# Performance work log

Measured on AMD Instinct MI355X. Metric: run time of the kernel, lower is better.

## Reference

```python
import jax, jax.numpy as jnp
import numpy as np

B, H, S, D = 4, 16, 2048, 128
D_MODEL = 128  # scale factor per module init


def setup_inputs() -> dict:
    key = jax.random.key(0)
    kq, kk, kv = jax.random.split(key, 3)
    Q = jax.random.normal(kq, (B, H, S, D), dtype=jnp.float32)
    K = jax.random.normal(kk, (B, H, S, D), dtype=jnp.float32)
    V = jax.random.normal(kv, (B, H, S, D), dtype=jnp.float32)
    return {"Q": Q, "K": K, "V": V}


def reference(Q, K, V):
    # scores: [B, H, S, S]
    scores = jnp.einsum("bhqd,bhkd->bhqk", Q, K) / np.sqrt(D_MODEL).astype(np.float32)
    # causal mask: lower-triangular keeps, upper becomes -inf
    q_idx = jnp.arange(S)[:, None]
    k_idx = jnp.arange(S)[None, :]
    causal = q_idx >= k_idx  # [S, S]
    scores = jnp.where(causal, scores, -jnp.inf)
    attn = jax.nn.softmax(scores, axis=-1)
    return jnp.einsum("bhqk,bhkd->bhqd", attn, V)
```

## Files before the change

kernel.cpp:

```cpp
#include <hip/hip_runtime.h>

typedef _Float16 f16;
typedef _Float16 f16x8 __attribute__((ext_vector_type(8)));
typedef float    f32x16 __attribute__((ext_vector_type(16)));
typedef int      i32x4 __attribute__((ext_vector_type(4)));

#define B_ 4
#define H_ 16
#define S_ 2048
#define D_ 128
#define KVB 32
#define KSTR 136
#define VTSTR 40

union U4 { i32x4 i; f16x8 h; };

__device__ __forceinline__ unsigned pk2(float a, float b) {
    auto v = __builtin_amdgcn_cvt_pkrtz(a, b);
    return __builtin_bit_cast(unsigned, v);
}

__device__ __forceinline__ f16x8 cvt8(const float4 a, const float4 b) {
    f16x8 h;
    h[0] = (f16)a.x; h[1] = (f16)a.y; h[2] = (f16)a.z; h[3] = (f16)a.w;
    h[4] = (f16)b.x; h[5] = (f16)b.y; h[6] = (f16)b.z; h[7] = (f16)b.w;
    return h;
}

__global__ __launch_bounds__(256)
void prep(const float* __restrict__ K, const float* __restrict__ V,
          f16* __restrict__ Kh, f16* __restrict__ Vtt)
{
    const int bid = blockIdx.x;
    const int bh  = bid >> 5;
    const int kb  = bid & 31;
    const int k0  = kb * 64;
    const int tid = threadIdx.x;

    const float* Kb = K + ((size_t)bh * S_ + k0) * D_;
    const float* Vb = V + ((size_t)bh * S_ + k0) * D_;
    f16* Khb = Kh + ((size_t)bh * S_ + k0) * D_;
    f16* Vtb = Vtt + (size_t)bh * S_ * D_ + (size_t)kb * 2 * (D_ * 32);

    #pragma unroll
    for (int it = 0; it < 4; ++it) {
        const int idx = tid + it * 256;
        const int row = idx >> 4, c8 = idx & 15;
        const float4 a = *(const float4*)(Kb + row * D_ + c8 * 8);
        const float4 b = *(const float4*)(Kb + row * D_ + c8 * 8 + 4);
        *(f16x8*)(Khb + row * D_ + c8 * 8) = cvt8(a, b);
    }
    #pragma unroll
    for (int it = 0; it < 4; ++it) {
        const int idx = tid + it * 256;
        const int d  = idx & 127;
        const int k8 = idx >> 7;
        const float* vp = Vb + (size_t)(k8 * 8) * D_ + d;
        f16x8 vh;
        #pragma unroll
        for (int e = 0; e < 8; ++e) vh[e] = (f16)vp[(size_t)e * D_];
        *(f16x8*)(Vtb + (size_t)(k8 >> 2) * (D_ * 32) + d * 32 + (k8 & 3) * 8) = vh;
    }
}

__global__ __launch_bounds__(256, 2)
void fattn10(const float* __restrict__ Qg, const f16* __restrict__ Khg,
             const f16* __restrict__ Vttg, float* __restrict__ Og)
{
    __shared__ __align__(16) f16 Klds[2][KVB * KSTR];
    __shared__ __align__(16) f16 Vt[2][128 * VTSTR];

    const int id  = blockIdx.x;
    const int xcd = id & 7;
    const int r   = id >> 3;
    const int bh  = xcd + 8 * (r & 7);
    const int p   = r >> 3;

    const int tid  = threadIdx.x;
    const int lane = tid & 63;
    const int l31  = lane & 31;
    const int h    = lane >> 5;
    const int wv   = tid >> 6;

    const float* Qb  = Qg   + (size_t)bh * S_ * D_;
    const f16*   Khb = Khg  + (size_t)bh * S_ * D_;
    const f16*   Vtb = Vttg + (size_t)bh * S_ * D_;
    float*       Ob  = Og   + (size_t)bh * S_ * D_;

    i32x4 kr[2], vr[2];
    auto issue = [&](int kt) {
        const int k0n = kt * KVB;
        #pragma unroll
        for (int it = 0; it < 2; ++it) {
            const int idx  = tid + it * 256;
            const int krow = idx >> 4, c8 = idx & 15;
            kr[it] = *(const i32x4*)(Khb + (size_t)(k0n + krow) * D_ + c8 * 8);
            vr[it] = *(const i32x4*)(Vtb + (size_t)kt * (D_ * 32) + (size_t)idx * 8);
        }
    };
    auto writeLds = [&](int buf) {
        #pragma unroll
        for (int it = 0; it < 2; ++it) {
            const int idx  = tid + it * 256;
            const int krow = idx >> 4, c8 = idx & 15;
            *(i32x4*)&Klds[buf][krow * KSTR + c8 * 8] = kr[it];
            const int d = idx >> 2, kk8 = idx & 3;
            *(i32x4*)&Vt[buf][d * VTSTR + kk8 * 8] = vr[it];
        }
    };
    f16x8 qf[8];
    auto qkt = [&](int buf) {
        f32x16 a;
        #pragma unroll
        for (int rr = 0; rr < 16; ++rr) a[rr] = 0.f;
        #pragma unroll
        for (int dc = 0; dc < 8; ++dc) {
            const f16x8 kf = *(const f16x8*)&Klds[buf][l31 * KSTR + dc * 16 + h * 8];
            a = __builtin_amdgcn_mfma_f32_32x32x16_f16(kf, qf[dc], a, 0, 0, 0);
        }
        return a;
    };

    const float qmul = 0.08838834764831845f * 1.4426950408889634f;

    #pragma unroll 1
    for (int ph = 0; ph < 2; ++ph) {
        const int qt  = ph ? 15 - p : p;
        const int qw0 = qt * 128 + wv * 32;
        const int qg  = qw0 + l31;
        const int nkt = 4 * qt + 4;

        issue(0);
        {
            const float* Qrow = Qb + (size_t)(qw0 + l31) * D_;
            #pragma unroll
            for (int dc = 0; dc < 8; ++dc) {
                const float4 a = *(const float4*)(Qrow + dc * 16 + h * 8);
                const float4 b = *(const float4*)(Qrow + dc * 16 + h * 8 + 4);
                f16x8 q;
                q[0] = (f16)(a.x * qmul); q[1] = (f16)(a.y * qmul);
                q[2] = (f16)(a.z * qmul); q[3] = (f16)(a.w * qmul);
                q[4] = (f16)(b.x * qmul); q[5] = (f16)(b.y * qmul);
                q[6] = (f16)(b.z * qmul); q[7] = (f16)(b.w * qmul);
                qf[dc] = q;
            }
        }

        f32x16 acc[4];
        #pragma unroll
        for (int dt = 0; dt < 4; ++dt)
            #pragma unroll
            for (int rr = 0; rr < 16; ++rr) acc[dt][rr] = 0.f;
        float m_i = -1e30f, l_i = 0.f;

        __syncthreads();
        writeLds(0);
        issue(1);
        __syncthreads();

        f32x16 sv = qkt(0);

        for (int kt = 0; kt < nkt; ++kt) {
            const int cur  = kt & 1;
            const bool more = (kt + 1 < nkt);

            if (more) {
                __syncthreads();
                writeLds(cur ^ 1);
                if (kt + 2 < nkt) issue(kt + 2);
                __syncthreads();
            }

            __builtin_amdgcn_s_setprio(1);
            f32x16 svn;
            if (more) svn = qkt(cur ^ 1);

            const int k0 = kt * KVB;
            if (k0 + 31 > qw0) {
                #pragma unroll
                for (int rr = 0; rr < 16; ++rr) {
                    const int kg = k0 + (rr & 3) + 8 * (rr >> 2) + 4 * h;
                    if (kg > qg) sv[rr] = -1e30f;
                }
            }
            float t[8];
            #pragma unroll
            for (int rr = 0; rr < 8; ++rr) t[rr] = fmaxf(sv[2 * rr], sv[2 * rr + 1]);
            #pragma unroll
            for (int rr = 0; rr < 4; ++rr) t[rr] = fmaxf(t[rr], t[rr + 4]);
            t[0] = fmaxf(t[0], t[2]); t[1] = fmaxf(t[1], t[3]);
            float mx = fmaxf(t[0], t[1]);
            mx = fmaxf(mx, __shfl_xor(mx, 32));
            if (!__all(mx - m_i <= 8.0f)) {
                const float mn = fmaxf(m_i, mx);
                const float al = exp2f(m_i - mn);
                m_i = mn;
                l_i *= al;
                float arow[16];
                #pragma unroll
                for (int rr = 0; rr < 16; ++rr)
                    arow[rr] = __shfl(al, (rr & 3) + 8 * (rr >> 2) + 4 * h);
                #pragma unroll
                for (int dt = 0; dt < 4; ++dt)
                    #pragma unroll
                    for (int rr = 0; rr < 16; ++rr) acc[dt][rr] *= arow[rr];
            }
            #pragma unroll
            for (int rr = 0; rr < 16; ++rr) sv[rr] = exp2f(sv[rr] - m_i);
            float s8[8];
            #pragma unroll
            for (int rr = 0; rr < 8; ++rr) s8[rr] = sv[2 * rr] + sv[2 * rr + 1];
            #pragma unroll
            for (int rr = 0; rr < 4; ++rr) s8[rr] += s8[rr + 4];
            s8[0] += s8[2]; s8[1] += s8[3];
            float rs = s8[0] + s8[1];
            rs += __shfl_xor(rs, 32);
            l_i += rs;
            U4 pa[2];
            {
                unsigned dwp[8];
                #pragma unroll
                for (int m = 0; m < 8; ++m) dwp[m] = pk2(sv[2 * m], sv[2 * m + 1]);
                #pragma unroll
                for (int hf = 0; hf < 2; ++hf) {
                    const unsigned a0 = dwp[hf * 4 + 0], a1 = dwp[hf * 4 + 1];
                    const unsigned b0 = dwp[hf * 4 + 2], b1 = dwp[hf * 4 + 3];
                    const unsigned sa0 = (unsigned)__shfl_xor((int)a0, 32);
                    const unsigned sa1 = (unsigned)__shfl_xor((int)a1, 32);
                    const unsigned sb0 = (unsigned)__shfl_xor((int)b0, 32);
                    const unsigned sb1 = (unsigned)__shfl_xor((int)b1, 32);
                    i32x4 d;
                    d[0] = h ? (int)sb0 : (int)a0;
                    d[1] = h ? (int)sb1 : (int)a1;
                    d[2] = h ? (int)b0  : (int)sa0;
                    d[3] = h ? (int)b1  : (int)sa1;
                    pa[hf].i = d;
                }
            }
            #pragma unroll
            for (int dt = 0; dt < 4; ++dt) {
                const f16* vrow = &Vt[cur][(dt * 32 + l31) * VTSTR + h * 8];
                const f16x8 vb0 = *(const f16x8*)(vrow + 0);
                const f16x8 vb1 = *(const f16x8*)(vrow + 16);
                acc[dt] = __builtin_amdgcn_mfma_f32_32x32x16_f16(pa[0].h, vb0, acc[dt], 0, 0, 0);
                acc[dt] = __builtin_amdgcn_mfma_f32_32x32x16_f16(pa[1].h, vb1, acc[dt], 0, 0, 0);
            }
            __builtin_amdgcn_s_setprio(0);

            if (more) sv = svn;
        }

        float li[16];
        #pragma unroll
        for (int rr = 0; rr < 16; ++rr) {
            const float lv = __shfl(l_i, (rr & 3) + 8 * (rr >> 2) + 4 * h);
            li[rr] = 1.0f / lv;
        }
        #pragma unroll
        for (int dt = 0; dt < 4; ++dt)
            #pragma unroll
            for (int rr = 0; rr < 16; ++rr) {
                const int row = qw0 + (rr & 3) + 8 * (rr >> 2) + 4 * h;
                Ob[(size_t)row * D_ + dt * 32 + l31] = acc[dt][rr] * li[rr];
            }
    }
}

__global__ __launch_bounds__(256, 3)
void fattn5(const float* __restrict__ Qg, const float* __restrict__ Kg,
            const float* __restrict__ Vg, float* __restrict__ Og)
{
    __shared__ __align__(16) f16 Klds[2][KVB * KSTR];
    __shared__ __align__(16) f16 Vt[2][128 * VTSTR];
    const int id  = blockIdx.x;
    const int xcd = id & 7;
    const int w   = id >> 3;
    const int qt  = 15 - (w & 15);
    const int bh  = xcd + 8 * (w >> 4);
    const int tid  = threadIdx.x;
    const int lane = tid & 63;
    const int wv   = tid >> 6;
    const int l31  = lane & 31;
    const int h    = lane >> 5;
    const int qw0 = qt * 128 + wv * 32;
    const int qg  = qw0 + l31;
    const size_t base = (size_t)bh * S_ * D_;
    const float* Qb = Qg + base;
    const float* Kb = Kg + base;
    const float* Vb = Vg + base;
    float*       Ob = Og + base;
    const int nkt = 4 * qt + 4;
    float4 kr[4];
    float  vr[16];
    auto issue = [&](int kt) {
        const int k0n = kt * KVB;
        #pragma unroll
        for (int it = 0; it < 2; ++it) {
            const int idx  = tid + it * 256;
            const int krow = idx >> 4;
            const int c8   = idx & 15;
            const float* kp = Kb + (size_t)(k0n + krow) * D_ + c8 * 8;
            kr[it * 2]     = *(const float4*)kp;
            kr[it * 2 + 1] = *(const float4*)(kp + 4);
            const int d  = idx & 127;
            const int k8 = idx >> 7;
            const float* vp = Vb + (size_t)(k0n + k8 * 8) * D_ + d;
            #pragma unroll
            for (int e = 0; e < 8; ++e) vr[it * 8 + e] = vp[(size_t)e * D_];
        }
    };
    auto writeLds = [&](int buf) {
        #pragma unroll
        for (int it = 0; it < 2; ++it) {
            const int idx  = tid + it * 256;
            const int krow = idx >> 4;
            const int c8   = idx & 15;
            *(f16x8*)&Klds[buf][krow * KSTR + c8 * 8] = cvt8(kr[it * 2], kr[it * 2 + 1]);
            const int d  = idx & 127;
            const int k8 = idx >> 7;
            f16x8 vh;
            #pragma unroll
            for (int e = 0; e < 8; ++e) vh[e] = (f16)vr[it * 8 + e];
            *(f16x8*)&Vt[buf][d * VTSTR + k8 * 8] = vh;
        }
    };
    const float qmul = 0.08838834764831845f * 1.4426950408889634f;
    f16x8 qf[8];
    {
        const float* Qrow = Qb + (size_t)(qw0 + l31) * D_;
        #pragma unroll
        for (int dc = 0; dc < 8; ++dc) {
            const float4 a = *(const float4*)(Qrow + dc * 16 + h * 8);
            const float4 b = *(const float4*)(Qrow + dc * 16 + h * 8 + 4);
            f16x8 q;
            q[0] = (f16)(a.x * qmul); q[1] = (f16)(a.y * qmul);
            q[2] = (f16)(a.z * qmul); q[3] = (f16)(a.w * qmul);
            q[4] = (f16)(b.x * qmul); q[5] = (f16)(b.y * qmul);
            q[6] = (f16)(b.z * qmul); q[7] = (f16)(b.w * qmul);
            qf[dc] = q;
        }
    }
    f32x16 acc[4];
    #pragma unroll
    for (int dt = 0; dt < 4; ++dt)
        #pragma unroll
        for (int rr = 0; rr < 16; ++rr) acc[dt][rr] = 0.f;
    float m_i = -1e30f, l_i = 0.f;
    issue(0);
    writeLds(0);
    if (nkt > 1) issue(1);
    __syncthreads();
    for (int kt = 0; kt < nkt; ++kt) {
        const int k0  = kt * KVB;
        const int cur = kt & 1;
        if (k0 <= qw0 + 31) {
            f32x16 sv;
            #pragma unroll
            for (int rr = 0; rr < 16; ++rr) sv[rr] = 0.f;
            #pragma unroll
            for (int dc = 0; dc < 8; ++dc) {
                const f16x8 kf = *(const f16x8*)&Klds[cur][l31 * KSTR + dc * 16 + h * 8];
                sv = __builtin_amdgcn_mfma_f32_32x32x16_f16(kf, qf[dc], sv, 0, 0, 0);
            }
            if (k0 + 31 > qw0) {
                #pragma unroll
                for (int rr = 0; rr < 16; ++rr) {
                    const int kg = k0 + (rr & 3) + 8 * (rr >> 2) + 4 * h;
                    if (kg > qg) sv[rr] = -1e30f;
                }
            }
            float mx = sv[0];
            #pragma unroll
            for (int rr = 1; rr < 16; ++rr) mx = fmaxf(mx, sv[rr]);
            mx = fmaxf(mx, __shfl_xor(mx, 32));
            if (!__all(mx - m_i <= 8.0f)) {
                const float mn = fmaxf(m_i, mx);
                const float al = exp2f(m_i - mn);
                m_i = mn;
                l_i *= al;
                float arow[16];
                #pragma unroll
                for (int rr = 0; rr < 16; ++rr)
                    arow[rr] = __shfl(al, (rr & 3) + 8 * (rr >> 2) + 4 * h);
                #pragma unroll
                for (int dt = 0; dt < 4; ++dt)
                    #pragma unroll
                    for (int rr = 0; rr < 16; ++rr) acc[dt][rr] *= arow[rr];
            }
            float rs = 0.f;
            #pragma unroll
            for (int rr = 0; rr < 16; ++rr) {
                sv[rr] = exp2f(sv[rr] - m_i);
                rs += sv[rr];
            }
            rs += __shfl_xor(rs, 32);
            l_i += rs;
            U4 pa[2];
            {
                unsigned dwp[8];
                #pragma unroll
                for (int m = 0; m < 8; ++m) dwp[m] = pk2(sv[2 * m], sv[2 * m + 1]);
                #pragma unroll
                for (int hf = 0; hf < 2; ++hf) {
                    const unsigned a0 = dwp[hf * 4 + 0], a1 = dwp[hf * 4 + 1];
                    const unsigned b0 = dwp[hf * 4 + 2], b1 = dwp[hf * 4 + 3];
                    const unsigned sa0 = (unsigned)__shfl_xor((int)a0, 32);
                    const unsigned sa1 = (unsigned)__shfl_xor((int)a1, 32);
                    const unsigned sb0 = (unsigned)__shfl_xor((int)b0, 32);
                    const unsigned sb1 = (unsigned)__shfl_xor((int)b1, 32);
                    i32x4 d;
                    d[0] = h ? (int)sb0 : (int)a0;
                    d[1] = h ? (int)sb1 : (int)a1;
                    d[2] = h ? (int)b0  : (int)sa0;
                    d[3] = h ? (int)b1  : (int)sa1;
                    pa[hf].i = d;
                }
            }
            #pragma unroll
            for (int dt = 0; dt < 4; ++dt) {
                const f16* vrow = &Vt[cur][(dt * 32 + l31) * VTSTR + h * 8];
                const f16x8 vb0 = *(const f16x8*)(vrow + 0);
                const f16x8 vb1 = *(const f16x8*)(vrow + 16);
                acc[dt] = __builtin_amdgcn_mfma_f32_32x32x16_f16(pa[0].h, vb0, acc[dt], 0, 0, 0);
                acc[dt] = __builtin_amdgcn_mfma_f32_32x32x16_f16(pa[1].h, vb1, acc[dt], 0, 0, 0);
            }
        }
        if (kt + 1 < nkt) {
            writeLds(cur ^ 1);
            if (kt + 2 < nkt) issue(kt + 2);
            __syncthreads();
        }
    }
    float li[16];
    #pragma unroll
    for (int rr = 0; rr < 16; ++rr) {
        const float lv = __shfl(l_i, (rr & 3) + 8 * (rr >> 2) + 4 * h);
        li[rr] = 1.0f / lv;
    }
    #pragma unroll
    for (int dt = 0; dt < 4; ++dt)
        #pragma unroll
        for (int rr = 0; rr < 16; ++rr) {
            const int row = qw0 + (rr & 3) + 8 * (rr >> 2) + 4 * h;
            Ob[(size_t)row * D_ + dt * 32 + l31] = acc[dt][rr] * li[rr];
        }
}

extern "C" void kernel_launch(void* const* d_in, const int* in_sizes, int n_in,
                              void* d_out, int out_size, void* d_ws, size_t ws_size,
                              hipStream_t stream) {
    (void)in_sizes; (void)n_in; (void)out_size;
    const float* Q = (const float*)d_in[0];
    const float* K = (const float*)d_in[1];
    const float* V = (const float*)d_in[2];
    float* O = (float*)d_out;
    const size_t elems  = (size_t)B_ * H_ * S_ * D_;
    const size_t needKV = elems * 2 * sizeof(f16);
    if (ws_size >= needKV) {
        f16* Kh  = (f16*)d_ws;
        f16* Vtt = Kh + elems;
        prep<<<dim3(B_ * H_ * (S_ / 64)), dim3(256), 0, stream>>>(K, V, Kh, Vtt);
        fattn10<<<dim3(512), dim3(256), 0, stream>>>(Q, Kh, Vtt, O);
    } else {
        fattn5<<<dim3((S_ / 128) * B_ * H_), dim3(256), 0, stream>>>(Q, K, V, O);
    }
}
```

Measured before the change: 160.9 us.

## Skip fully masked causal tiles per wave and raise occupancy target

Each wave now works out the last KV tile its 32 query rows can see. It skips the QK^T MFMA and the whole softmax/PV block for tiles beyond that, while still taking part in the shared LDS loads and barriers. Launch bounds go from 2 to 3 blocks per SM, load and store addressing is precomputed outside the loop, the max reduction is reshaped into 3-input fmax chains, and the Q load loop is only partly unrolled to relieve register pressure. The aim is to drop wasted masked-tile work and improve latency hiding, at the risk of register spills under the tighter occupancy bound.

```diff
diff --git a/kernel.cpp b/kernel.cpp
--- a/kernel.cpp
+++ b/kernel.cpp
@@ -63,8 +63,8 @@
     }
 }
 
-__global__ __launch_bounds__(256, 2)
-void fattn10(const float* __restrict__ Qg, const f16* __restrict__ Khg,
+__global__ __launch_bounds__(256, 3)
+void fattn11(const float* __restrict__ Qg, const f16* __restrict__ Khg,
              const f16* __restrict__ Vttg, float* __restrict__ Og)
 {
     __shared__ __align__(16) f16 Klds[2][KVB * KSTR];
@@ -87,26 +87,27 @@
     const f16*   Vtb = Vttg + (size_t)bh * S_ * D_;
     float*       Ob  = Og   + (size_t)bh * S_ * D_;
 
+    const f16* kS = Khb + (tid >> 4) * D_ + (tid & 15) * 8;
+    const f16* vS = Vtb + (size_t)tid * 8;
+    const int  kDo = (tid >> 4) * KSTR + (tid & 15) * 8;
+    const int  vDo = (tid >> 2) * VTSTR + (tid & 3) * 8;
+
     i32x4 kr[2], vr[2];
     auto issue = [&](int kt) {
-        const int k0n = kt * KVB;
-        #pragma unroll
-        for (int it = 0; it < 2; ++it) {
-            const int idx  = tid + it * 256;
-            const int krow = idx >> 4, c8 = idx & 15;
-            kr[it] = *(const i32x4*)(Khb + (size_t)(k0n + krow) * D_ + c8 * 8);
-            vr[it] = *(const i32x4*)(Vtb + (size_t)kt * (D_ * 32) + (size_t)idx * 8);
-        }
+        const f16* kp = kS + ((size_t)kt << 12);
+        const f16* vp = vS + ((size_t)kt << 12);
+        kr[0] = *(const i32x4*)kp;
+        kr[1] = *(const i32x4*)(kp + 2048);
+        vr[0] = *(const i32x4*)vp;
+        vr[1] = *(const i32x4*)(vp + 2048);
     };
     auto writeLds = [&](int buf) {
-        #pragma unroll
-        for (int it = 0; it < 2; ++it) {
-            const int idx  = tid + it * 256;
-            const int krow = idx >> 4, c8 = idx & 15;
-            *(i32x4*)&Klds[buf][krow * KSTR + c8 * 8] = kr[it];
-            const int d = idx >> 2, kk8 = idx & 3;
-            *(i32x4*)&Vt[buf][d * VTSTR + kk8 * 8] = vr[it];
-        }
+        f16* kb = &Klds[buf][0];
+        f16* vb = &Vt[buf][0];
+        *(i32x4*)(kb + kDo)             = kr[0];
+        *(i32x4*)(kb + kDo + 16 * KSTR) = kr[1];
+        *(i32x4*)(vb + vDo)             = vr[0];
+        *(i32x4*)(vb + vDo + 64 * VTSTR) = vr[1];
     };
     f16x8 qf[8];
     auto qkt = [&](int buf) {
@@ -129,11 +130,12 @@
         const int qw0 = qt * 128 + wv * 32;
         const int qg  = qw0 + l31;
         const int nkt = 4 * qt + 4;
+        const int lastt = 4 * qt + wv;
 
         issue(0);
         {
             const float* Qrow = Qb + (size_t)(qw0 + l31) * D_;
-            #pragma unroll
+            #pragma unroll 2
             for (int dc = 0; dc < 8; ++dc) {
                 const float4 a = *(const float4*)(Qrow + dc * 16 + h * 8);
                 const float4 b = *(const float4*)(Qrow + dc * 16 + h * 8 + 4);
@@ -173,77 +175,80 @@
 
             __builtin_amdgcn_s_setprio(1);
             f32x16 svn;
-            if (more) svn = qkt(cur ^ 1);
-
-            const int k0 = kt * KVB;
-            if (k0 + 31 > qw0) {
-                #pragma unroll
-                for (int rr = 0; rr < 16; ++rr) {
-                    const int kg = k0 + (rr & 3) + 8 * (rr >> 2) + 4 * h;
-                    if (kg > qg) sv[rr] = -1e30f;
-                }
-            }
-            float t[8];
-            #pragma unroll
-            for (int rr = 0; rr < 8; ++rr) t[rr] = fmaxf(sv[2 * rr], sv[2 * rr + 1]);
-            #pragma unroll
-            for (int rr = 0; rr < 4; ++rr) t[rr] = fmaxf(t[rr], t[rr + 4]);
-            t[0] = fmaxf(t[0], t[2]); t[1] = fmaxf(t[1], t[3]);
-            float mx = fmaxf(t[0], t[1]);
-            mx = fmaxf(mx, __shfl_xor(mx, 32));
-            if (!__all(mx - m_i <= 8.0f)) {
-                const float mn = fmaxf(m_i, mx);
-                const float al = exp2f(m_i - mn);
-                m_i = mn;
-                l_i *= al;
-                float arow[16];
-                #pragma unroll
-                for (int rr = 0; rr < 16; ++rr)
-                    arow[rr] = __shfl(al, (rr & 3) + 8 * (rr >> 2) + 4 * h);
-                #pragma unroll
-                for (int dt = 0; dt < 4; ++dt)
-                    #pragma unroll
-                    for (int rr = 0; rr < 16; ++rr) acc[dt][rr] *= arow[rr];
-            }
-            #pragma unroll
-            for (int rr = 0; rr < 16; ++rr) sv[rr] = exp2f(sv[rr] - m_i);
-            float s8[8];
-            #pragma unroll
-            for (int rr = 0; rr < 8; ++rr) s8[rr] = sv[2 * rr] + sv[2 * rr + 1];
-            #pragma unroll
-            for (int rr = 0; rr < 4; ++rr) s8[rr] += s8[rr + 4];
-            s8[0] += s8[2]; s8[1] += s8[3];
-            float rs = s8[0] + s8[1];
-            rs += __shfl_xor(rs, 32);
-            l_i += rs;
-            U4 pa[2];
-            {
-                unsigned dwp[8];
-                #pragma unroll
-                for (int m = 0; m < 8; ++m) dwp[m] = pk2(sv[2 * m], sv[2 * m + 1]);
-                #pragma unroll
-                for (int hf = 0; hf < 2; ++hf) {
-                    const unsigned a0 = dwp[hf * 4 + 0], a1 = dwp[hf * 4 + 1];
-                    const unsigned b0 = dwp[hf * 4 + 2], b1 = dwp[hf * 4 + 3];
-                    const unsigned sa0 = (unsigned)__shfl_xor((int)a0, 32);
-                    const unsigned sa1 = (unsigned)__shfl_xor((int)a1, 32);
-                    const unsigned sb0 = (unsigned)__shfl_xor((int)b0, 32);
-                    const unsigned sb1 = (unsigned)__shfl_xor((int)b1, 32);
-                    i32x4 d;
-                    d[0] = h ? (int)sb0 : (int)a0;
-                    d[1] = h ? (int)sb1 : (int)a1;
-                    d[2] = h ? (int)b0  : (int)sa0;
-                    d[3] = h ? (int)b1  : (int)sa1;
-                    pa[hf].i = d;
-                }
-            }
-            #pragma unroll
-            for (int dt = 0; dt < 4; ++dt) {
-                const f16* vrow = &Vt[cur][(dt * 32 + l31) * VTSTR + h * 8];
-                const f16x8 vb0 = *(const f16x8*)(vrow + 0);
-                const f16x8 vb1 = *(const f16x8*)(vrow + 16);
-                acc[dt] = __builtin_amdgcn_mfma_f32_32x32x16_f16(pa[0].h, vb0, acc[dt], 0, 0, 0);
-                acc[dt] = __builtin_amdgcn_mfma_f32_32x32x16_f16(pa[1].h, vb1, acc[dt], 0, 0, 0);
+            if (more && kt + 1 <= lastt) svn = qkt(cur ^ 1);
+
+            if (kt <= lastt) {
+                const int k0 = kt * KVB;
+                if (k0 + 31 > qw0) {
+                    #pragma unroll
+                    for (int rr = 0; rr < 16; ++rr) {
+                        const int kg = k0 + (rr & 3) + 8 * (rr >> 2) + 4 * h;
+                        if (kg > qg) sv[rr] = -1e30f;
+                    }
+                }
+                const float m1 = fmaxf(fmaxf(sv[0], sv[1]), sv[2]);
+                const float m2 = fmaxf(fmaxf(sv[3], sv[4]), sv[5]);
+                const float m3 = fmaxf(fmaxf(sv[6], sv[7]), sv[8]);
+                const float m4 = fmaxf(fmaxf(sv[9], sv[10]), sv[11]);
+                const float m5 = fmaxf(fmaxf(sv[12], sv[13]), sv[14]);
+                float mx = fmaxf(fmaxf(m1, m2), m3);
+                mx = fmaxf(fmaxf(mx, m4), m5);
+                mx = fmaxf(mx, sv[15]);
+                mx = fmaxf(mx, __shfl_xor(mx, 32));
+                if (!__all(mx - m_i <= 8.0f)) {
+                    const float mn = fmaxf(m_i, mx);
+                    const float al = exp2f(m_i - mn);
+                    m_i = mn;
+                    l_i *= al;
+                    float arow[16];
+                    #pragma unroll
+                    for (int rr = 0; rr < 16; ++rr)
+                        arow[rr] = __shfl(al, (rr & 3) + 8 * (rr >> 2) + 4 * h);
+                    #pragma unroll
+                    for (int dt = 0; dt < 4; ++dt)
+                        #pragma unroll
+                        for (int rr = 0; rr < 16; ++rr) acc[dt][rr] *= arow[rr];
+                }
+                #pragma unroll
+                for (int rr = 0; rr < 16; ++rr) sv[rr] = exp2f(sv[rr] - m_i);
+                float s8[8];
+                #pragma unroll
+                for (int rr = 0; rr < 8; ++rr) s8[rr] = sv[2 * rr] + sv[2 * rr + 1];
+                #pragma unroll
+                for (int rr = 0; rr < 4; ++rr) s8[rr] += s8[rr + 4];
+                s8[0] += s8[2]; s8[1] += s8[3];
+                float rs = s8[0] + s8[1];
+                rs += __shfl_xor(rs, 32);
+                l_i += rs;
+                U4 pa[2];
+                {
+                    unsigned dwp[8];
+                    #pragma unroll
+                    for (int m = 0; m < 8; ++m) dwp[m] = pk2(sv[2 * m], sv[2 * m + 1]);
+                    #pragma unroll
+                    for (int hf = 0; hf < 2; ++hf) {
+                        const unsigned a0 = dwp[hf * 4 + 0], a1 = dwp[hf * 4 + 1];
+                        const unsigned b0 = dwp[hf * 4 + 2], b1 = dwp[hf * 4 + 3];
+                        const unsigned sa0 = (unsigned)__shfl_xor((int)a0, 32);
+                        const unsigned sa1 = (unsigned)__shfl_xor((int)a1, 32);
+                        const unsigned sb0 = (unsigned)__shfl_xor((int)b0, 32);
+                        const unsigned sb1 = (unsigned)__shfl_xor((int)b1, 32);
+                        i32x4 d;
+                        d[0] = h ? (int)sb0 : (int)a0;
+                        d[1] = h ? (int)sb1 : (int)a1;
+                        d[2] = h ? (int)b0  : (int)sa0;
+                        d[3] = h ? (int)b1  : (int)sa1;
+                        pa[hf].i = d;
+                    }
+                }
+                #pragma unroll
+                for (int dt = 0; dt < 4; ++dt) {
+                    const f16* vrow = &Vt[cur][(dt * 32 + l31) * VTSTR + h * 8];
+                    const f16x8 vb0 = *(const f16x8*)(vrow + 0);
+                    const f16x8 vb1 = *(const f16x8*)(vrow + 16);
+                    acc[dt] = __builtin_amdgcn_mfma_f32_32x32x16_f16(pa[0].h, vb0, acc[dt], 0, 0, 0);
+                    acc[dt] = __builtin_amdgcn_mfma_f32_32x32x16_f16(pa[1].h, vb1, acc[dt], 0, 0, 0);
+                }
             }
             __builtin_amdgcn_s_setprio(0);
 
@@ -460,7 +465,7 @@
         f16* Kh  = (f16*)d_ws;
         f16* Vtt = Kh + elems;
         prep<<<dim3(B_ * H_ * (S_ / 64)), dim3(256), 0, stream>>>(K, V, Kh, Vtt);
-        fattn10<<<dim3(512), dim3(256), 0, stream>>>(Q, Kh, Vtt, O);
+        fattn11<<<dim3(512), dim3(256), 0, stream>>>(Q, Kh, Vtt, O);
     } else {
         fattn5<<<dim3((S_ / 128) * B_ * H_), dim3(256), 0, stream>>>(Q, K, V, O);
     }
```

Result: slower. 331.8 us (+106.2%).
